# Kernel optimization log

Measured on AMD Instinct MI355X. Metric: run time of the kernel, lower is better.

The kernel has to match this reference:

```python
import jax, jax.numpy as jnp
import numpy as np

IN_FEATURES = 1024
OUT_FEATURES = 256
BATCH = 131072
EPS = 1e-4


def setup_inputs() -> dict:
    key = jax.random.key(0)
    kx, kw, kb = jax.random.split(key, 3)
    x = jax.random.normal(kx, (BATCH, IN_FEATURES), dtype=jnp.float32)
    # nn.Linear default init: U(-1/sqrt(in), 1/sqrt(in)) for both W and b
    bound = 1.0 / np.sqrt(IN_FEATURES)
    W = jax.random.uniform(kw, (OUT_FEATURES, IN_FEATURES), dtype=jnp.float32, minval=-bound, maxval=bound)
    b = jax.random.uniform(kb, (OUT_FEATURES,), dtype=jnp.float32, minval=-bound, maxval=bound)
    return {"x": x, "W": W, "b": b}


def reference(x, W, b):
    # L2-normalize each row (dim=1), matching x / (||x||_2 + 1e-4)
    norm = jnp.sqrt(jnp.sum(x * x, axis=1, keepdims=True))
    x_dir = x / (norm + EPS)
    # Linear: x_dir @ W^T + b, then ReLU
    h = jnp.einsum('bi,oi->bo', x_dir, W) + b
    return jax.nn.relu(h)
```

## Files before the change

### kernel.cpp

```cpp
#include <hip/hip_runtime.h>


#define IN_F   1024
#define OUT_F  256
#define BATCH  131072
#define BM     128
#define NKT    32
#define EPSV   1e-4f

typedef __attribute__((ext_vector_type(8))) __bf16 bf16x8;
typedef __attribute__((ext_vector_type(4))) __bf16 bf16x4;
typedef __attribute__((ext_vector_type(4))) float  f32x4;

__device__ __forceinline__ void gload_lds16(const void* g, void* lds) {
  __builtin_amdgcn_global_load_lds(
      (const __attribute__((address_space(1))) void*)g,
      (__attribute__((address_space(3))) void*)lds, 16, 0, 0);
}

#define VM_WAIT(N) do { asm volatile("s_waitcnt vmcnt(" #N ")" ::: "memory"); \
                        __builtin_amdgcn_sched_barrier(0); } while (0)

__global__ void wconv_kernel(const float* __restrict__ W, __bf16* __restrict__ Wb) {
  const int t = blockIdx.x * blockDim.x + threadIdx.x;
  const float4 v = reinterpret_cast<const float4*>(W)[t];
  bf16x4 h;
  h[0] = (__bf16)v.x; h[1] = (__bf16)v.y; h[2] = (__bf16)v.z; h[3] = (__bf16)v.w;
  reinterpret_cast<bf16x4*>(Wb)[t] = h;
}

__global__ __launch_bounds__(1024, 4)
void ffl_kernel(const float* __restrict__ x, const __bf16* __restrict__ Wb,
                const float* __restrict__ bias, float* __restrict__ out) {
  __shared__ __align__(16) char smem[163840];
  char* const Ab[3] = {smem, smem + 32768, smem + 65536};
  char* const Bb[4] = {smem + 98304, smem + 114688, smem + 131072, smem + 147456};

  const int tid  = threadIdx.x;
  const int lane = tid & 63;
  const int wave = tid >> 6;
  const int wr   = wave >> 2;
  const int wc   = wave & 3;
  const int rm   = lane & 15;
  const int q    = lane >> 4;
  const size_t block_row = (size_t)blockIdx.x * BM;
  const int phg = blockIdx.x & 15;

  const float* aSrc[2]; int aDst[2];
  #pragma unroll
  for (int i = 0; i < 2; ++i) {
    const int c   = 2 * wave + i;
    const int row = 4 * c + (lane >> 4);
    const int s   = (lane & 15) ^ (row & 7);
    aSrc[i] = x + (block_row + row) * IN_F + s * 4;
    aDst[i] = c * 1024;
  }
  const int brow = 16 * wave + (lane >> 2);
  const int bs   = (lane & 3) ^ ((brow >> 1) & 3);
  const __bf16* bSrc = Wb + (size_t)brow * IN_F + bs * 8;
  const int bDst = wave * 1024;

  f32x4 acc[2][4];
  #pragma unroll
  for (int m = 0; m < 2; ++m)
    #pragma unroll
    for (int n = 0; n < 4; ++n)
      acc[m][n] = (f32x4){0.f, 0.f, 0.f, 0.f};

  float ssq0 = 0.f, ssq1 = 0.f;

  auto stageA = [&](int g) {
    const int pg = (g + phg) & 15;
    gload_lds16(aSrc[0] + pg * 64, Ab[g % 3] + aDst[0]);
    gload_lds16(aSrc[1] + pg * 64, Ab[g % 3] + aDst[1]);
  };
  auto stageB = [&](int kt) {
    const int pk = (kt + 2 * phg) & 31;
    gload_lds16(bSrc + pk * 32, Bb[kt & 3] + bDst);
  };

  stageA(0);
  stageA(1);
  stageB(0);
  stageB(1);
  stageB(2);
  VM_WAIT(2);
  __builtin_amdgcn_s_barrier();

  #pragma unroll
  for (int kt = 0; kt < NKT; ++kt) {
    if (kt + 3 < NKT) stageB(kt + 3);
    if ((kt & 1) == 0 && (kt / 2 + 2) < 16) stageA(kt / 2 + 2);

    const char* abuf = Ab[(kt >> 1) % 3];
    const char* bbuf = Bb[kt & 3];
    const int   gb   = (kt & 1) * 8 + 2 * q;

    bf16x8 aF[2];
    #pragma unroll
    for (int m = 0; m < 2; ++m) {
      const int ra = wr * 32 + m * 16 + rm;
      const char* ab = abuf + ra * 256;
      const int sw = ra & 7;
      const f32x4 lo = *reinterpret_cast<const f32x4*>(ab + ((gb)     ^ sw) * 16);
      const f32x4 hi = *reinterpret_cast<const f32x4*>(ab + ((gb + 1) ^ sw) * 16);
      float& ssq = m ? ssq1 : ssq0;
      ssq += lo[0]*lo[0] + lo[1]*lo[1] + lo[2]*lo[2] + lo[3]*lo[3]
           + hi[0]*hi[0] + hi[1]*hi[1] + hi[2]*hi[2] + hi[3]*hi[3];
      bf16x8 a;
      a[0]=(__bf16)lo[0]; a[1]=(__bf16)lo[1]; a[2]=(__bf16)lo[2]; a[3]=(__bf16)lo[3];
      a[4]=(__bf16)hi[0]; a[5]=(__bf16)hi[1]; a[6]=(__bf16)hi[2]; a[7]=(__bf16)hi[3];
      aF[m] = a;
    }

    #pragma unroll
    for (int n = 0; n < 4; ++n) {
      const int rb = wc * 64 + n * 16 + rm;
      const bf16x8 bF = *reinterpret_cast<const bf16x8*>(
          bbuf + rb * 64 + (q ^ ((rb >> 1) & 3)) * 16);
      acc[0][n] = __builtin_amdgcn_mfma_f32_16x16x32_bf16(aF[0], bF, acc[0][n], 0, 0, 0);
      acc[1][n] = __builtin_amdgcn_mfma_f32_16x16x32_bf16(aF[1], bF, acc[1][n], 0, 0, 0);
    }

    if (kt == 29)                              { VM_WAIT(1); }
    else if (kt >= 30)                         { VM_WAIT(0); }
    else if (kt == 0 || kt == 28 || (kt & 1))  { VM_WAIT(4); }
    else                                       { VM_WAIT(6); }
    __builtin_amdgcn_s_barrier();
  }

  ssq0 += __shfl_xor(ssq0, 16); ssq0 += __shfl_xor(ssq0, 32);
  ssq1 += __shfl_xor(ssq1, 16); ssq1 += __shfl_xor(ssq1, 32);
  float* norms = reinterpret_cast<float*>(smem + 163328);
  if (wc == 0 && q == 0) {
    norms[wr * 32 + rm]      = 1.0f / (sqrtf(ssq0) + EPSV);
    norms[wr * 32 + 16 + rm] = 1.0f / (sqrtf(ssq1) + EPSV);
  }
  __syncthreads();

  float* stg = reinterpret_cast<float*>(smem);
  const int col0 = wc * 64 + rm;
  #pragma unroll
  for (int n = 0; n < 4; ++n) {
    const float bn = bias[col0 + n * 16];
    #pragma unroll
    for (int m = 0; m < 2; ++m) {
      #pragma unroll
      for (int j = 0; j < 4; ++j) {
        const int lr = wr * 32 + m * 16 + q * 4 + j;
        stg[lr * 260 + col0 + n * 16] = fmaxf(acc[m][n][j] * norms[lr] + bn, 0.f);
      }
    }
  }
  __syncthreads();

  const int r = tid >> 3, p = tid & 7;
  const float* srow = stg + r * 260;
  float* orow = out + (block_row + r) * OUT_F;
  #pragma unroll
  for (int i = 0; i < 8; ++i) {
    const int f = i * 8 + p;
    const f32x4 v = *reinterpret_cast<const f32x4*>(srow + f * 4);
    *reinterpret_cast<f32x4*>(orow + f * 4) = v;
  }
}

extern "C" void kernel_launch(void* const* d_in, const int* in_sizes, int n_in,
                              void* d_out, int out_size, void* d_ws, size_t ws_size,
                              hipStream_t stream) {
  const float* x = (const float*)d_in[0];
  const float* W = (const float*)d_in[1];
  const float* b = (const float*)d_in[2];
  float* out = (float*)d_out;
  __bf16* Wb = (__bf16*)d_ws;

  wconv_kernel<<<(OUT_F * IN_F / 4) / 256, 256, 0, stream>>>(W, Wb);
  ffl_kernel<<<BATCH / BM, 1024, 0, stream>>>(x, Wb, b, out);
}
```

Measured before the change: 170.6 us.

## Halve row tile to 64 and remap waves to 2x8 layout

Shrinks the per-block row tile from 128 to 64, doubling the grid and re-partitioning the 16 waves into 2 row groups by 8 column groups, each computing 32 columns. The A staging now loads 512-byte rows with wider K chunks per stage, spreading the two A loads across iterations, and the wait counts are re-tuned to match. The aim is more blocks for better load balance and latency hiding. The cost is that each W tile is reused across fewer rows, raising W LDS traffic per output.

```diff
diff --git a/kernel.cpp b/kernel.cpp
--- a/kernel.cpp
+++ b/kernel.cpp
@@ -4,7 +4,7 @@
 #define IN_F   1024
 #define OUT_F  256
 #define BATCH  131072
-#define BM     128
+#define BM     64
 #define NKT    32
 #define EPSV   1e-4f
 
@@ -39,20 +39,20 @@
   const int tid  = threadIdx.x;
   const int lane = tid & 63;
   const int wave = tid >> 6;
-  const int wr   = wave >> 2;
-  const int wc   = wave & 3;
+  const int wr   = wave >> 3;
+  const int wcn  = wave & 7;
   const int rm   = lane & 15;
   const int q    = lane >> 4;
   const size_t block_row = (size_t)blockIdx.x * BM;
-  const int phg = blockIdx.x & 15;
+  const int phg = blockIdx.x & 7;
 
   const float* aSrc[2]; int aDst[2];
   #pragma unroll
   for (int i = 0; i < 2; ++i) {
     const int c   = 2 * wave + i;
-    const int row = 4 * c + (lane >> 4);
-    const int s   = (lane & 15) ^ (row & 7);
-    aSrc[i] = x + (block_row + row) * IN_F + s * 4;
+    const int row = 2 * c + (lane >> 5);
+    const int gs  = (lane & 31) ^ (row & 7);
+    aSrc[i] = x + (block_row + row) * IN_F + gs * 4;
     aDst[i] = c * 1024;
   }
   const int brow = 16 * wave + (lane >> 2);
@@ -60,50 +60,54 @@
   const __bf16* bSrc = Wb + (size_t)brow * IN_F + bs * 8;
   const int bDst = wave * 1024;
 
-  f32x4 acc[2][4];
+  f32x4 acc[2][2];
   #pragma unroll
   for (int m = 0; m < 2; ++m)
     #pragma unroll
-    for (int n = 0; n < 4; ++n)
+    for (int n = 0; n < 2; ++n)
       acc[m][n] = (f32x4){0.f, 0.f, 0.f, 0.f};
 
   float ssq0 = 0.f, ssq1 = 0.f;
 
-  auto stageA = [&](int g) {
-    const int pg = (g + phg) & 15;
-    gload_lds16(aSrc[0] + pg * 64, Ab[g % 3] + aDst[0]);
-    gload_lds16(aSrc[1] + pg * 64, Ab[g % 3] + aDst[1]);
+  auto stageAinst = [&](int g, int i) {
+    const int pg = (g + phg) & 7;
+    gload_lds16(aSrc[i] + pg * 128, Ab[g % 3] + aDst[i]);
   };
   auto stageB = [&](int kt) {
-    const int pk = (kt + 2 * phg) & 31;
+    const int pk = (kt + 4 * phg) & 31;
     gload_lds16(bSrc + pk * 32, Bb[kt & 3] + bDst);
   };
 
-  stageA(0);
-  stageA(1);
+  stageAinst(0, 0); stageAinst(0, 1);
   stageB(0);
+  stageAinst(1, 0); stageAinst(1, 1);
   stageB(1);
   stageB(2);
-  VM_WAIT(2);
+  VM_WAIT(4);
   __builtin_amdgcn_s_barrier();
 
   #pragma unroll
   for (int kt = 0; kt < NKT; ++kt) {
+    const int g = kt >> 2, r = kt & 3;
+
     if (kt + 3 < NKT) stageB(kt + 3);
-    if ((kt & 1) == 0 && (kt / 2 + 2) < 16) stageA(kt / 2 + 2);
+    if (g + 2 <= 7) {
+      if (r == 0)      stageAinst(g + 2, 0);
+      else if (r == 1) stageAinst(g + 2, 1);
+    }
 
-    const char* abuf = Ab[(kt >> 1) % 3];
+    const char* abuf = Ab[g % 3];
     const char* bbuf = Bb[kt & 3];
-    const int   gb   = (kt & 1) * 8 + 2 * q;
+    const int   r8g  = r * 8;
 
     bf16x8 aF[2];
     #pragma unroll
     for (int m = 0; m < 2; ++m) {
       const int ra = wr * 32 + m * 16 + rm;
-      const char* ab = abuf + ra * 256;
+      const char* ab = abuf + ra * 512;
       const int sw = ra & 7;
-      const f32x4 lo = *reinterpret_cast<const f32x4*>(ab + ((gb)     ^ sw) * 16);
-      const f32x4 hi = *reinterpret_cast<const f32x4*>(ab + ((gb + 1) ^ sw) * 16);
+      const f32x4 lo = *reinterpret_cast<const f32x4*>(ab + ((r8g + 2 * q)     ^ sw) * 16);
+      const f32x4 hi = *reinterpret_cast<const f32x4*>(ab + ((r8g + 2 * q + 1) ^ sw) * 16);
       float& ssq = m ? ssq1 : ssq0;
       ssq += lo[0]*lo[0] + lo[1]*lo[1] + lo[2]*lo[2] + lo[3]*lo[3]
            + hi[0]*hi[0] + hi[1]*hi[1] + hi[2]*hi[2] + hi[3]*hi[3];
@@ -114,34 +118,35 @@
     }
 
     #pragma unroll
-    for (int n = 0; n < 4; ++n) {
-      const int rb = wc * 64 + n * 16 + rm;
+    for (int n = 0; n < 2; ++n) {
+      const int rb = wcn * 32 + n * 16 + rm;
       const bf16x8 bF = *reinterpret_cast<const bf16x8*>(
           bbuf + rb * 64 + (q ^ ((rb >> 1) & 3)) * 16);
       acc[0][n] = __builtin_amdgcn_mfma_f32_16x16x32_bf16(aF[0], bF, acc[0][n], 0, 0, 0);
       acc[1][n] = __builtin_amdgcn_mfma_f32_16x16x32_bf16(aF[1], bF, acc[1][n], 0, 0, 0);
     }
 
-    if (kt == 29)                              { VM_WAIT(1); }
-    else if (kt >= 30)                         { VM_WAIT(0); }
-    else if (kt == 0 || kt == 28 || (kt & 1))  { VM_WAIT(4); }
-    else                                       { VM_WAIT(6); }
+    if (kt >= 30)                            { VM_WAIT(0); }
+    else if (kt == 29)                       { VM_WAIT(1); }
+    else if (kt >= 24)                       { VM_WAIT(2); }
+    else if ((kt & 3) == 1 || (kt & 3) == 2) { VM_WAIT(4); }
+    else                                     { VM_WAIT(3); }
     __builtin_amdgcn_s_barrier();
   }
 
   ssq0 += __shfl_xor(ssq0, 16); ssq0 += __shfl_xor(ssq0, 32);
   ssq1 += __shfl_xor(ssq1, 16); ssq1 += __shfl_xor(ssq1, 32);
-  float* norms = reinterpret_cast<float*>(smem + 163328);
-  if (wc == 0 && q == 0) {
+  float* norms = reinterpret_cast<float*>(smem + 163456);
+  if (wcn == 0 && q == 0) {
     norms[wr * 32 + rm]      = 1.0f / (sqrtf(ssq0) + EPSV);
     norms[wr * 32 + 16 + rm] = 1.0f / (sqrtf(ssq1) + EPSV);
   }
   __syncthreads();
 
   float* stg = reinterpret_cast<float*>(smem);
-  const int col0 = wc * 64 + rm;
+  const int col0 = wcn * 32 + rm;
   #pragma unroll
-  for (int n = 0; n < 4; ++n) {
+  for (int n = 0; n < 2; ++n) {
     const float bn = bias[col0 + n * 16];
     #pragma unroll
     for (int m = 0; m < 2; ++m) {
@@ -154,12 +159,12 @@
   }
   __syncthreads();
 
-  const int r = tid >> 3, p = tid & 7;
-  const float* srow = stg + r * 260;
-  float* orow = out + (block_row + r) * OUT_F;
+  const int rr = tid >> 4, p = tid & 15;
+  const float* srow = stg + rr * 260;
+  float* orow = out + (block_row + rr) * OUT_F;
   #pragma unroll
-  for (int i = 0; i < 8; ++i) {
-    const int f = i * 8 + p;
+  for (int i = 0; i < 4; ++i) {
+    const int f = i * 16 + p;
     const f32x4 v = *reinterpret_cast<const f32x4*>(srow + f * 4);
     *reinterpret_cast<f32x4*>(orow + f * 4) = v;
   }
```

New measurement: 196.0 us. 1.15x slower.
